# Kernel tuning notes

Hardware: AMD Instinct MI355X
Metric: run time of the kernel (lower is better)

## Reference

```python
import jax, jax.numpy as jnp
import numpy as np

TEMPERATURE = 8.0   # sqrt(d_k), d_k = 64
TOP_K = 5           # SparseAttention default top_k in mimicry/RIMs
EPS = 1e-7          # matches torch 10e-8


def _sparsify(attn_rows):
    """Per-row top-k sparsification: keep mass above the k-th largest value,
    clamp at zero, renormalize. attn_rows: [N, L]."""
    topk_vals = jax.lax.top_k(attn_rows, TOP_K)[0]          # [N, K]
    delta = topk_vals[:, -1:] + EPS                          # k-th largest per row
    w = jnp.maximum(attn_rows - delta, 0.0)                  # clamp(min=0)
    return w / (jnp.sum(w, axis=1, keepdims=True) + EPS)


def setup_inputs() -> dict:
    key = jax.random.key(0)
    kq, kk, kv = jax.random.split(key, 3)
    B, L, D = 4, 4096, 64
    q = jax.random.normal(kq, (B, L, D), dtype=jnp.float32)
    k = jax.random.normal(kk, (B, L, D), dtype=jnp.float32)
    v = jax.random.normal(kv, (B, L, D), dtype=jnp.float32)
    return {"q": q, "k": k, "v": v}


def reference(q, k, v):
    # attn = softmax(q k^T / temperature); dropout is identity in eval mode
    attn = jnp.einsum('bqd,bkd->bqk', q / TEMPERATURE, k)   # [B, Lq, Lk]
    attn = jax.nn.softmax(attn, axis=-1)
    B, Lq, Lk = attn.shape
    attn = _sparsify(attn.reshape(B * Lq, Lk)).reshape(B, Lq, Lk)
    out = jnp.einsum('bqk,bkd->bqd', attn, v)               # [B, Lq, Dv]
    return out, attn
```

## Files before the change

kernel.cpp:

```cpp
#include <hip/hip_runtime.h>
#include <math.h>

#define NB 4
#define L 4096
#define D 64
#define WS_K  1048576
#define KBS   262144
#define QSCALE 0.1803368801111243f

typedef __attribute__((ext_vector_type(8))) short short8;
typedef __attribute__((ext_vector_type(4))) float floatx4;

static __device__ inline unsigned short f2bf(float x) {
    unsigned int u = __builtin_bit_cast(unsigned int, x);
    return (unsigned short)((u + (0x7FFFu + ((u >> 16) & 1u))) >> 16);
}

__global__ __launch_bounds__(256)
void convert_kernel(const float* __restrict__ qg, const float* __restrict__ kg,
                    unsigned short* __restrict__ ws) {
    unsigned int i = blockIdx.x * 256 + threadIdx.x;
    if (i < 262144) {
        float4 qv = ((const float4*)qg)[i];
        ushort4 h;
        h.x = f2bf(qv.x * QSCALE); h.y = f2bf(qv.y * QSCALE);
        h.z = f2bf(qv.z * QSCALE); h.w = f2bf(qv.w * QSCALE);
        *(ushort4*)&ws[i * 4] = h;
    } else {
        unsigned int j = i - 262144;
        float4 kv = ((const float4*)kg)[j];
        ushort4 h;
        h.x = f2bf(kv.x); h.y = f2bf(kv.y); h.z = f2bf(kv.z); h.w = f2bf(kv.w);
        unsigned int bcol = j >> 4;
        unsigned int f4   = j & 15;
        unsigned int b    = bcol >> 12, col = bcol & 4095;
        unsigned int cq   = f4 >> 1, half = f4 & 1;
        size_t base = WS_K + (size_t)b * KBS + ((size_t)cq * 4096 + col) * 8 + half * 4;
        *(ushort4*)&ws[base] = h;
    }
}

static __device__ inline void ins5(float d[5], float t) {
    float n0 = fmaxf(d[0], t);
    float n1 = __builtin_amdgcn_fmed3f(t, d[0], d[1]);
    float n2 = __builtin_amdgcn_fmed3f(t, d[1], d[2]);
    float n3 = __builtin_amdgcn_fmed3f(t, d[2], d[3]);
    float n4 = __builtin_amdgcn_fmed3f(t, d[3], d[4]);
    d[0] = n0; d[1] = n1; d[2] = n2; d[3] = n3; d[4] = n4;
}

static __device__ inline void merge8(float d[8], const float o[8]) {
#pragma unroll
    for (int j = 0; j < 8; ++j) {
        float t = o[j];
        float carry = d[j];
        d[j] = fmaxf(d[j], t);
#pragma unroll
        for (int k = j + 1; k < 8; ++k) {
            float pk = d[k];
            d[k] = __builtin_amdgcn_fmed3f(t, carry, d[k]);
            carry = pk;
        }
    }
}

__global__ __launch_bounds__(512, 4)
void sparse_attn_kernel(const unsigned short* __restrict__ ws,
                        const float* __restrict__ qg,
                        const float* __restrict__ kg,
                        const float* __restrict__ vg,
                        float* __restrict__ outg) {
    __shared__ float smv[2][4][16][8];

    const int tid  = threadIdx.x;
    const int lane = tid & 63;
    const int wid  = tid >> 6;
    const int cq   = wid & 3;
    const int rh   = wid >> 2;
    const int c16  = lane & 15;
    const int quad = lane >> 4;

    const int sblk  = (blockIdx.x & 7) * 64 + (blockIdx.x >> 3);
    const int qbase = sblk * 32;
    const int qbw   = qbase + rh * 16;
    const int b     = qbase >> 12;
    const int phase = sblk & 63;

    const unsigned short* qh   = ws;
    const unsigned short* kbat = ws + WS_K + (size_t)b * KBS;
    const float* vb = vg + (size_t)b * L * D;
    float* attng = outg + (size_t)NB * L * D;

    const int qrow = qbw + c16;
    const short8 a0h = *(const short8*)&qh[(size_t)qrow * 64 + quad * 8];
    const short8 a1h = *(const short8*)&qh[(size_t)qrow * 64 + 32 + quad * 8];

    float tv[5];
#pragma unroll
    for (int i = 0; i < 5; ++i) tv[i] = -INFINITY;

    const int colq = cq * 1024;
    const unsigned short* bp0 = kbat + ((size_t)(quad)     * 4096 + colq + c16) * 8;
    const unsigned short* bp1 = kbat + ((size_t)(4 + quad) * 4096 + colq + c16) * 8;
    const float4 zv = make_float4(0.f, 0.f, 0.f, 0.f);

    const int colb0 = colq + quad * 4;

#pragma unroll 4
    for (int cg0 = 0; cg0 < 64; ++cg0) {
        int cg = cg0 + phase;
        cg = (cg >= 64) ? cg - 64 : cg;

        const int off = cg * 128;
        short8 b0h = *(const short8*)(bp0 + off);
        short8 b1h = *(const short8*)(bp1 + off);
        floatx4 acc = {0.f, 0.f, 0.f, 0.f};
        acc = __builtin_amdgcn_mfma_f32_16x16x32_bf16(b0h, a0h, acc, 0, 0, 0);
        acc = __builtin_amdgcn_mfma_f32_16x16x32_bf16(b1h, a1h, acc, 0, 0, 0);

        {
            int idx = cg * 64 + lane;
            *(float4*)&attng[(size_t)(qbw + (idx >> 8)) * L + colq + (idx & 255) * 4] = zv;
        }

        const int cxb = (colb0 + cg * 16) ^ 4095;
#pragma unroll
        for (int r = 0; r < 4; ++r) {
            int si  = __builtin_bit_cast(int, (float)acc[r]);
            int tag = (cxb ^ r) ^ ((si >> 31) & 4095);
            int ti  = (si & 0xFFFFF000) | tag;
            ins5(tv, __builtin_bit_cast(float, ti));
        }
    }

    float e[8];
#pragma unroll
    for (int i = 0; i < 5; ++i) e[i] = tv[i];
#pragma unroll
    for (int i = 5; i < 8; ++i) e[i] = -INFINITY;
#pragma unroll
    for (int m = 16; m <= 32; m <<= 1) {
        float o[8];
#pragma unroll
        for (int i = 0; i < 8; ++i) o[i] = __shfl_xor(e[i], m, 64);
        merge8(e, o);
    }

    if (quad == 0) {
#pragma unroll
        for (int i = 0; i < 8; ++i) smv[rh][cq][c16][i] = e[i];
    }
    __syncthreads();

    if (cq == 0) {
#pragma unroll
        for (int r = 0; r < 4; ++r) {
            const int rowl = quad * 4 + r;
            float lv[8];
#pragma unroll
            for (int i = 0; i < 8; ++i) lv[i] = smv[rh][0][rowl][i];
#pragma unroll
            for (int f = 1; f < 4; ++f) {
                float o[8];
#pragma unroll
                for (int i = 0; i < 8; ++i) o[i] = smv[rh][f][rowl][i];
                merge8(lv, o);
            }

            unsigned int ic[8];
#pragma unroll
            for (int j = 0; j < 8; ++j) {
                int t = __builtin_bit_cast(int, lv[j]);
                ic[j] = (unsigned)((t & 4095) ^ (t >= 0 ? 4095 : 0));
            }

            const int rowabs = qbw + rowl;

            const float4 qv = *(const float4*)(qg + (size_t)rowabs * D + c16 * 4);
            float s[8];
#pragma unroll
            for (int j = 0; j < 8; ++j) {
                const float4 kv = *(const float4*)(kg + ((size_t)(b * L) + ic[j]) * D + c16 * 4);
                float p = qv.x * kv.x + qv.y * kv.y + qv.z * kv.z + qv.w * kv.w;
                p += __shfl_xor(p, 1, 64);
                p += __shfl_xor(p, 2, 64);
                p += __shfl_xor(p, 4, 64);
                p += __shfl_xor(p, 8, 64);
                s[j] = p * QSCALE;
            }

#pragma unroll
            for (int j = 0; j < 5; ++j)
#pragma unroll
                for (int k = j + 1; k < 8; ++k) {
                    bool sw = s[k] > s[j];
                    float ts = sw ? s[k] : s[j];
                    s[k] = sw ? s[j] : s[k];  s[j] = ts;
                    unsigned int tc2 = sw ? ic[k] : ic[j];
                    ic[k] = sw ? ic[j] : ic[k]; ic[j] = tc2;
                }

            float u0 = fmaxf(exp2f(s[0] - s[4]) - 1.0f, 0.0f);
            float u1 = fmaxf(exp2f(s[1] - s[4]) - 1.0f, 0.0f);
            float u2 = fmaxf(exp2f(s[2] - s[4]) - 1.0f, 0.0f);
            float u3 = fmaxf(exp2f(s[3] - s[4]) - 1.0f, 0.0f);
            float inv = 1.0f / (u0 + u1 + u2 + u3 + 1e-30f);
            float w0 = u0 * inv, w1 = u1 * inv, w2 = u2 * inv, w3 = u3 * inv;

            const float4 v0 = *(const float4*)(vb + (size_t)ic[0] * D + c16 * 4);
            const float4 v1 = *(const float4*)(vb + (size_t)ic[1] * D + c16 * 4);
            const float4 v2 = *(const float4*)(vb + (size_t)ic[2] * D + c16 * 4);
            const float4 v3 = *(const float4*)(vb + (size_t)ic[3] * D + c16 * 4);
            float4 o;
            o.x = w0 * v0.x + w1 * v1.x + w2 * v2.x + w3 * v3.x;
            o.y = w0 * v0.y + w1 * v1.y + w2 * v2.y + w3 * v3.y;
            o.z = w0 * v0.z + w1 * v1.z + w2 * v2.z + w3 * v3.z;
            o.w = w0 * v0.w + w1 * v1.w + w2 * v2.w + w3 * v3.w;
            *(float4*)(outg + (size_t)rowabs * D + c16 * 4) = o;

            if (c16 < 4) {
                float wv = c16 == 0 ? w0 : c16 == 1 ? w1 : c16 == 2 ? w2 : w3;
                unsigned int cs = ic[c16];
                if (wv > 0.f)
                    attng[(size_t)rowabs * L + cs] = wv;
            }
        }
    }
}

extern "C" void kernel_launch(void* const* d_in, const int* in_sizes, int n_in,
                              void* d_out, int out_size, void* d_ws, size_t ws_size,
                              hipStream_t stream) {
    const float* q = (const float*)d_in[0];
    const float* k = (const float*)d_in[1];
    const float* v = (const float*)d_in[2];
    float* out = (float*)d_out;
    unsigned short* ws = (unsigned short*)d_ws;

    convert_kernel<<<2048, 256, 0, stream>>>(q, k, ws);

    sparse_attn_kernel<<<512, 512, 0, stream>>>(ws, q, k, v, out);
}
```

Measured before the change: 322.8 us.

## Split each block over 16 query rows with 8 column-slice waves

Each block now handles 16 query rows instead of 32, and all 8 waves split the 4096 key columns into 512-column slices, so the grid doubles to 1024 blocks with a higher occupancy hint. The final merge and gather stage now uses 4 waves, each taking one row per quad, instead of one wave looping over 4 rows. K-row dot products are batched four at a time to expose more memory-level parallelism. The aim is better latency hiding and shorter per-wave serial work, at the cost of merging 8 partial top-k lists per row and sharing fewer Q loads per block.

Result: faster. 295.3 us, median of 2 (-8.5%).

```diff
diff --git a/kernel.cpp b/kernel.cpp
--- a/kernel.cpp
+++ b/kernel.cpp
@@ -64,34 +64,31 @@
     }
 }
 
-__global__ __launch_bounds__(512, 4)
+__global__ __launch_bounds__(512, 8)
 void sparse_attn_kernel(const unsigned short* __restrict__ ws,
                         const float* __restrict__ qg,
                         const float* __restrict__ kg,
                         const float* __restrict__ vg,
                         float* __restrict__ outg) {
-    __shared__ float smv[2][4][16][8];
+    __shared__ float smv[8][16][8];
 
     const int tid  = threadIdx.x;
     const int lane = tid & 63;
     const int wid  = tid >> 6;
-    const int cq   = wid & 3;
-    const int rh   = wid >> 2;
     const int c16  = lane & 15;
     const int quad = lane >> 4;
 
-    const int sblk  = (blockIdx.x & 7) * 64 + (blockIdx.x >> 3);
-    const int qbase = sblk * 32;
-    const int qbw   = qbase + rh * 16;
+    const int sblk  = (blockIdx.x & 7) * 128 + (blockIdx.x >> 3);
+    const int qbase = sblk * 16;
     const int b     = qbase >> 12;
-    const int phase = sblk & 63;
+    const int phase = sblk & 31;
 
     const unsigned short* qh   = ws;
     const unsigned short* kbat = ws + WS_K + (size_t)b * KBS;
     const float* vb = vg + (size_t)b * L * D;
     float* attng = outg + (size_t)NB * L * D;
 
-    const int qrow = qbw + c16;
+    const int qrow = qbase + c16;
     const short8 a0h = *(const short8*)&qh[(size_t)qrow * 64 + quad * 8];
     const short8 a1h = *(const short8*)&qh[(size_t)qrow * 64 + 32 + quad * 8];
 
@@ -99,17 +96,16 @@
 #pragma unroll
     for (int i = 0; i < 5; ++i) tv[i] = -INFINITY;
 
-    const int colq = cq * 1024;
+    const int colq = wid * 512;
     const unsigned short* bp0 = kbat + ((size_t)(quad)     * 4096 + colq + c16) * 8;
     const unsigned short* bp1 = kbat + ((size_t)(4 + quad) * 4096 + colq + c16) * 8;
     const float4 zv = make_float4(0.f, 0.f, 0.f, 0.f);
-
     const int colb0 = colq + quad * 4;
 
-#pragma unroll 4
-    for (int cg0 = 0; cg0 < 64; ++cg0) {
+#pragma unroll 2
+    for (int cg0 = 0; cg0 < 32; ++cg0) {
         int cg = cg0 + phase;
-        cg = (cg >= 64) ? cg - 64 : cg;
+        cg = (cg >= 32) ? cg - 32 : cg;
 
         const int off = cg * 128;
         short8 b0h = *(const short8*)(bp0 + off);
@@ -120,7 +116,7 @@
 
         {
             int idx = cg * 64 + lane;
-            *(float4*)&attng[(size_t)(qbw + (idx >> 8)) * L + colq + (idx & 255) * 4] = zv;
+            *(float4*)&attng[(size_t)(qbase + (idx >> 7)) * L + colq + (idx & 127) * 4] = zv;
         }
 
         const int cxb = (colb0 + cg * 16) ^ 4095;
@@ -148,82 +144,91 @@
 
     if (quad == 0) {
 #pragma unroll
-        for (int i = 0; i < 8; ++i) smv[rh][cq][c16][i] = e[i];
+        for (int i = 0; i < 8; ++i) smv[wid][c16][i] = e[i];
     }
     __syncthreads();
 
-    if (cq == 0) {
-#pragma unroll
-        for (int r = 0; r < 4; ++r) {
-            const int rowl = quad * 4 + r;
-            float lv[8];
-#pragma unroll
-            for (int i = 0; i < 8; ++i) lv[i] = smv[rh][0][rowl][i];
-#pragma unroll
-            for (int f = 1; f < 4; ++f) {
-                float o[8];
-#pragma unroll
-                for (int i = 0; i < 8; ++i) o[i] = smv[rh][f][rowl][i];
-                merge8(lv, o);
+    if (wid < 4) {
+        const int rowl = quad * 4 + wid;
+        float lv[8];
+#pragma unroll
+        for (int i = 0; i < 8; ++i) lv[i] = smv[0][rowl][i];
+#pragma unroll
+        for (int f = 1; f < 8; ++f) {
+            float o[8];
+#pragma unroll
+            for (int i = 0; i < 8; ++i) o[i] = smv[f][rowl][i];
+            merge8(lv, o);
+        }
+
+        unsigned int ic[8];
+#pragma unroll
+        for (int j = 0; j < 8; ++j) {
+            int t = __builtin_bit_cast(int, lv[j]);
+            ic[j] = (unsigned)((t & 4095) ^ (t >= 0 ? 4095 : 0));
+        }
+
+        const int rowabs = qbase + rowl;
+
+        const float4 qv = *(const float4*)(qg + (size_t)rowabs * D + c16 * 4);
+        float s[8];
+#pragma unroll
+        for (int batch = 0; batch < 2; ++batch) {
+            float4 kv0 = *(const float4*)(kg + ((size_t)(b * L) + ic[batch * 4 + 0]) * D + c16 * 4);
+            float4 kv1 = *(const float4*)(kg + ((size_t)(b * L) + ic[batch * 4 + 1]) * D + c16 * 4);
+            float4 kv2 = *(const float4*)(kg + ((size_t)(b * L) + ic[batch * 4 + 2]) * D + c16 * 4);
+            float4 kv3 = *(const float4*)(kg + ((size_t)(b * L) + ic[batch * 4 + 3]) * D + c16 * 4);
+            float p0 = qv.x * kv0.x + qv.y * kv0.y + qv.z * kv0.z + qv.w * kv0.w;
+            float p1 = qv.x * kv1.x + qv.y * kv1.y + qv.z * kv1.z + qv.w * kv1.w;
+            float p2 = qv.x * kv2.x + qv.y * kv2.y + qv.z * kv2.z + qv.w * kv2.w;
+            float p3 = qv.x * kv3.x + qv.y * kv3.y + qv.z * kv3.z + qv.w * kv3.w;
+#pragma unroll
+            for (int m = 1; m <= 8; m <<= 1) {
+                p0 += __shfl_xor(p0, m, 64);
+                p1 += __shfl_xor(p1, m, 64);
+                p2 += __shfl_xor(p2, m, 64);
+                p3 += __shfl_xor(p3, m, 64);
             }
-
-            unsigned int ic[8];
-#pragma unroll
-            for (int j = 0; j < 8; ++j) {
-                int t = __builtin_bit_cast(int, lv[j]);
-                ic[j] = (unsigned)((t & 4095) ^ (t >= 0 ? 4095 : 0));
+            s[batch * 4 + 0] = p0 * QSCALE;
+            s[batch * 4 + 1] = p1 * QSCALE;
+            s[batch * 4 + 2] = p2 * QSCALE;
+            s[batch * 4 + 3] = p3 * QSCALE;
+        }
+
+#pragma unroll
+        for (int j = 0; j < 5; ++j)
+#pragma unroll
+            for (int k = j + 1; k < 8; ++k) {
+                bool sw = s[k] > s[j];
+                float ts = sw ? s[k] : s[j];
+                s[k] = sw ? s[j] : s[k];  s[j] = ts;
+                unsigned int tc2 = sw ? ic[k] : ic[j];
+                ic[k] = sw ? ic[j] : ic[k]; ic[j] = tc2;
             }
 
-            const int rowabs = qbw + rowl;
-
-            const float4 qv = *(const float4*)(qg + (size_t)rowabs * D + c16 * 4);
-            float s[8];
-#pragma unroll
-            for (int j = 0; j < 8; ++j) {
-                const float4 kv = *(const float4*)(kg + ((size_t)(b * L) + ic[j]) * D + c16 * 4);
-                float p = qv.x * kv.x + qv.y * kv.y + qv.z * kv.z + qv.w * kv.w;
-                p += __shfl_xor(p, 1, 64);
-                p += __shfl_xor(p, 2, 64);
-                p += __shfl_xor(p, 4, 64);
-                p += __shfl_xor(p, 8, 64);
-                s[j] = p * QSCALE;
-            }
-
-#pragma unroll
-            for (int j = 0; j < 5; ++j)
-#pragma unroll
-                for (int k = j + 1; k < 8; ++k) {
-                    bool sw = s[k] > s[j];
-                    float ts = sw ? s[k] : s[j];
-                    s[k] = sw ? s[j] : s[k];  s[j] = ts;
-                    unsigned int tc2 = sw ? ic[k] : ic[j];
-                    ic[k] = sw ? ic[j] : ic[k]; ic[j] = tc2;
-                }
-
-            float u0 = fmaxf(exp2f(s[0] - s[4]) - 1.0f, 0.0f);
-            float u1 = fmaxf(exp2f(s[1] - s[4]) - 1.0f, 0.0f);
-            float u2 = fmaxf(exp2f(s[2] - s[4]) - 1.0f, 0.0f);
-            float u3 = fmaxf(exp2f(s[3] - s[4]) - 1.0f, 0.0f);
-            float inv = 1.0f / (u0 + u1 + u2 + u3 + 1e-30f);
-            float w0 = u0 * inv, w1 = u1 * inv, w2 = u2 * inv, w3 = u3 * inv;
-
-            const float4 v0 = *(const float4*)(vb + (size_t)ic[0] * D + c16 * 4);
-            const float4 v1 = *(const float4*)(vb + (size_t)ic[1] * D + c16 * 4);
-            const float4 v2 = *(const float4*)(vb + (size_t)ic[2] * D + c16 * 4);
-            const float4 v3 = *(const float4*)(vb + (size_t)ic[3] * D + c16 * 4);
-            float4 o;
-            o.x = w0 * v0.x + w1 * v1.x + w2 * v2.x + w3 * v3.x;
-            o.y = w0 * v0.y + w1 * v1.y + w2 * v2.y + w3 * v3.y;
-            o.z = w0 * v0.z + w1 * v1.z + w2 * v2.z + w3 * v3.z;
-            o.w = w0 * v0.w + w1 * v1.w + w2 * v2.w + w3 * v3.w;
-            *(float4*)(outg + (size_t)rowabs * D + c16 * 4) = o;
-
-            if (c16 < 4) {
-                float wv = c16 == 0 ? w0 : c16 == 1 ? w1 : c16 == 2 ? w2 : w3;
-                unsigned int cs = ic[c16];
-                if (wv > 0.f)
-                    attng[(size_t)rowabs * L + cs] = wv;
-            }
+        float u0 = fmaxf(exp2f(s[0] - s[4]) - 1.0f, 0.0f);
+        float u1 = fmaxf(exp2f(s[1] - s[4]) - 1.0f, 0.0f);
+        float u2 = fmaxf(exp2f(s[2] - s[4]) - 1.0f, 0.0f);
+        float u3 = fmaxf(exp2f(s[3] - s[4]) - 1.0f, 0.0f);
+        float inv = 1.0f / (u0 + u1 + u2 + u3 + 1e-30f);
+        float w0 = u0 * inv, w1 = u1 * inv, w2 = u2 * inv, w3 = u3 * inv;
+
+        const float4 v0 = *(const float4*)(vb + (size_t)ic[0] * D + c16 * 4);
+        const float4 v1 = *(const float4*)(vb + (size_t)ic[1] * D + c16 * 4);
+        const float4 v2 = *(const float4*)(vb + (size_t)ic[2] * D + c16 * 4);
+        const float4 v3 = *(const float4*)(vb + (size_t)ic[3] * D + c16 * 4);
+        float4 o;
+        o.x = w0 * v0.x + w1 * v1.x + w2 * v2.x + w3 * v3.x;
+        o.y = w0 * v0.y + w1 * v1.y + w2 * v2.y + w3 * v3.y;
+        o.z = w0 * v0.z + w1 * v1.z + w2 * v2.z + w3 * v3.z;
+        o.w = w0 * v0.w + w1 * v1.w + w2 * v2.w + w3 * v3.w;
+        *(float4*)(outg + (size_t)rowabs * D + c16 * 4) = o;
+
+        if (c16 < 4) {
+            float wv = c16 == 0 ? w0 : c16 == 1 ? w1 : c16 == 2 ? w2 : w3;
+            unsigned int cs = ic[c16];
+            if (wv > 0.f)
+                attng[(size_t)rowabs * L + cs] = wv;
         }
     }
 }
@@ -239,5 +244,5 @@
 
     convert_kernel<<<2048, 256, 0, stream>>>(q, k, ws);
 
-    sparse_attn_kernel<<<512, 512, 0, stream>>>(ws, q, k, v, out);
-}
+    sparse_attn_kernel<<<1024, 512, 0, stream>>>(ws, q, k, v, out);
+}
```
